# Optimization experiments

Measured on AMD Instinct MI355X. Metric: run time of the kernel, lower is better.

Reference implementation:

```python
import jax, jax.numpy as jnp
import numpy as np

POOL_K = {56: 8, 28: 4, 14: 2, 7: 1}


def _maxpool(x, k):
    # kernel == stride maxpool via reshape-max
    if k == 1:
        return x
    B, C, H, W = x.shape
    return x.reshape(B, C, H // k, k, W // k, k).max(axis=(3, 5))


def _scale(act):
    # act: [B, C, H0, W0] -> pooled [B, C, 7, 7]
    B, C, H0, W0 = act.shape
    p = _maxpool(act, POOL_K[H0]).reshape(B, C, -1)  # [B, C, HW], HW=49
    # heatmap[i,j,e,f] = sum_c p[i,c,e] * p[j,c,f]  -> [B, B, HW, HW]
    heat = jax.nn.softmax(jnp.einsum('ice,jcf->ijef', p, p), axis=-1)
    # out[i,j,e,c] = sum_f heat[i,j,e,f] * p[j,c,f]  -> [B, B, HW, C]
    out = jnp.einsum('ijef,jcf->ijec', heat, p)
    return out, heat


def setup_inputs() -> dict:
    key = jax.random.key(0)
    k1, k2, k3, k4 = jax.random.split(key, 4)
    B = 16
    return {
        'act1': jax.random.normal(k1, (B, 256, 56, 56), dtype=jnp.float32),
        'act2': jax.random.normal(k2, (B, 512, 28, 28), dtype=jnp.float32),
        'act3': jax.random.normal(k3, (B, 1024, 14, 14), dtype=jnp.float32),
        'act4': jax.random.normal(k4, (B, 2048, 7, 7), dtype=jnp.float32),
    }


def reference(act1, act2, act3, act4):
    outs_heats = [_scale(a) for a in (act1, act2, act3, act4)]
    outs = tuple(o for o, _ in outs_heats)
    heats = tuple(h for _, h in outs_heats)
    return outs + heats
```

## Files before the change

### kernel.cpp

```cpp
#include <hip/hip_runtime.h>
#include <hip/hip_bf16.h>
#include <cstdint>
#include <cstddef>


typedef __attribute__((ext_vector_type(8))) short s16x8;
typedef __attribute__((ext_vector_type(4))) float f32x4;

#define SPART 802816

__device__ __forceinline__ unsigned short f2bf(float x) {
    uint32_t u = __float_as_uint(x);
    uint32_t r = (u + 0x7fff + ((u >> 16) & 1)) >> 16;
    return (unsigned short)r;
}
__device__ __forceinline__ float bf2f(unsigned short b) {
    return __uint_as_float(((uint32_t)b) << 16);
}
__device__ __forceinline__ void gll16(const void* g, void* l) {
    __builtin_amdgcn_global_load_lds(
        (const __attribute__((address_space(1))) uint32_t*)g,
        (__attribute__((address_space(3))) uint32_t*)l, 16, 0, 0);
}

__global__ __launch_bounds__(256) void pool_kernel(const float* __restrict__ act,
                                                   unsigned short* __restrict__ Pk,
                                                   unsigned short* __restrict__ Pk2,
                                                   unsigned short* __restrict__ Vb,
                                                   int C, int H, int k, int G) {
    __shared__ float plane[3136];
    const int HW = H * H;
    const int nblk_c = C / G;
    const int i  = blockIdx.x / nblk_c;
    const int c0 = (blockIdx.x % nblk_c) * G;
    const float* src = act + ((size_t)i * C + c0) * HW;
    for (int idx = threadIdx.x; idx < G * HW; idx += 256)
        plane[idx] = src[idx];
    __syncthreads();
    for (int idx = threadIdx.x; idx < G * 49; idx += 256) {
        const int e = idx / G, g = idx % G;
        const int eh = e / 7, ew = e % 7;
        const float* pp = plane + g * HW + (eh * k) * H + ew * k;
        float m = -INFINITY;
        for (int dy = 0; dy < k; ++dy)
            for (int dx = 0; dx < k; ++dx)
                m = fmaxf(m, pp[dy * H + dx]);
        const int c = c0 + g;
        const unsigned short hb = f2bf(m);
        const unsigned short lb = f2bf(m - bf2f(hb));
        const size_t pk = (((size_t)(c >> 2) * 896) + (size_t)i * 56 + e) * 8 + ((c & 3) * 2);
        *reinterpret_cast<uint32_t*>(&Pk[pk])  = (uint32_t)hb | ((uint32_t)lb << 16);
        *reinterpret_cast<uint32_t*>(&Pk2[pk]) = (uint32_t)lb | ((uint32_t)hb << 16);
        const size_t vb = (((size_t)i * 8 + (e >> 3)) * C + c) * 8 + (e & 7);
        Vb[vb] = hb;
    }
    for (int idx = threadIdx.x; idx < 7 * G; idx += 256) {
        const int e = 49 + idx / G, g = idx % G, c = c0 + g;
        const size_t pk = (((size_t)(c >> 2) * 896) + (size_t)i * 56 + e) * 8 + ((c & 3) * 2);
        *reinterpret_cast<uint32_t*>(&Pk[pk])  = 0;
        *reinterpret_cast<uint32_t*>(&Pk2[pk]) = 0;
    }
    for (int idx = threadIdx.x; idx < 15 * G; idx += 256) {
        const int e = 49 + idx / G, g = idx % G, c = c0 + g;
        const size_t vb = (((size_t)i * 8 + (e >> 3)) * C + c) * 8 + (e & 7);
        Vb[vb] = 0;
    }
}

struct GramParams {
    const unsigned short* Pk[4];
    const unsigned short* Pk2[4];
    float* S[4];
    int Kblk[4];
    int cum[5];
};

__global__ __launch_bounds__(256) void gram_kernel(GramParams g) {
    __shared__ short lsA[4 * 128 * 8];
    __shared__ short lsB[4 * 128 * 8];
    __shared__ short lsB2[4 * 128 * 8];
    int b = blockIdx.x, s = 0;
    while (b >= g.cum[s + 1]) s++;
    const int rem = b - g.cum[s];
    const int p = rem / 49, t = rem % 49;
    const int bi = t / 7, bj = t % 7;
    const int Kb = g.Kblk[s];
    const int kg0 = p * (Kb >> 3);
    const unsigned short* __restrict__ Pk  = g.Pk[s];
    const unsigned short* __restrict__ Pk2 = g.Pk2[s];
    float* __restrict__ S = g.S[s] + (size_t)p * SPART;

    const int tid = threadIdx.x, lane = tid & 63, w = tid >> 6;
    const int wm = (w >> 1) * 64, wn = (w & 1) * 64;

    f32x4 acc[4][4];
    #pragma unroll
    for (int u = 0; u < 4; ++u)
        #pragma unroll
        for (int v = 0; v < 4; ++v)
            acc[u][v] = (f32x4){0.f, 0.f, 0.f, 0.f};

    const int half = lane >> 4, r16 = lane & 15;
    for (int it = 0; it < (Kb >> 5); ++it) {
        const int kq = kg0 + it * 4 + w;
        const char* ga  = (const char*)Pk  + ((size_t)kq * 896 + bi * 128) * 16 + lane * 16;
        const char* gb  = (const char*)Pk  + ((size_t)kq * 896 + bj * 128) * 16 + lane * 16;
        const char* gb2 = (const char*)Pk2 + ((size_t)kq * 896 + bj * 128) * 16 + lane * 16;
        gll16(ga,         (char*)lsA  + w * 2048);
        gll16(ga  + 1024, (char*)lsA  + w * 2048 + 1024);
        gll16(gb,         (char*)lsB  + w * 2048);
        gll16(gb  + 1024, (char*)lsB  + w * 2048 + 1024);
        gll16(gb2,        (char*)lsB2 + w * 2048);
        gll16(gb2 + 1024, (char*)lsB2 + w * 2048 + 1024);
        __syncthreads();
        s16x8 av[4], bv[4], cv[4];
        #pragma unroll
        for (int u = 0; u < 4; ++u) {
            av[u] = *reinterpret_cast<const s16x8*>(&lsA [((half * 128) + wm + 16 * u + r16) * 8]);
            bv[u] = *reinterpret_cast<const s16x8*>(&lsB [((half * 128) + wn + 16 * u + r16) * 8]);
            cv[u] = *reinterpret_cast<const s16x8*>(&lsB2[((half * 128) + wn + 16 * u + r16) * 8]);
        }
        #pragma unroll
        for (int u = 0; u < 4; ++u)
            #pragma unroll
            for (int v = 0; v < 4; ++v) {
                acc[u][v] = __builtin_amdgcn_mfma_f32_16x16x32_bf16(av[u], bv[v], acc[u][v], 0, 0, 0);
                acc[u][v] = __builtin_amdgcn_mfma_f32_16x16x32_bf16(av[u], cv[v], acc[u][v], 0, 0, 0);
            }
        __syncthreads();
    }

    const int rowb = bi * 128 + wm + (lane >> 4) * 4;
    const int colb = bj * 128 + wn + (lane & 15);
    #pragma unroll
    for (int u = 0; u < 4; ++u)
        #pragma unroll
        for (int v = 0; v < 4; ++v)
            #pragma unroll
            for (int rg = 0; rg < 4; ++rg)
                S[(size_t)(rowb + 16 * u + rg) * 896 + colb + 16 * v] = acc[u][v][rg];
}

struct SoftParams {
    const float* S[4];
    float* heat[4];
    unsigned short* Hb[4];
    int np[4];
};

__global__ __launch_bounds__(256) void softmax_kernel(SoftParams sp) {
    const int grp = (blockIdx.x * 256 + threadIdx.x) >> 4;
    const int l = threadIdx.x & 15;
    const int s = grp / 12544;
    const int rem = grp % 12544;
    const int i = rem / 784;
    const int j = (rem / 49) % 16;
    const int e = rem % 49;
    const float* __restrict__ Sb = sp.S[s];
    const int np = sp.np[s];
    const size_t rowoff = ((size_t)(i * 56 + e)) * 896 + j * 56;

    float v[4];
    #pragma unroll
    for (int t = 0; t < 4; ++t) {
        const int f = l + t * 16;
        float x = -INFINITY;
        if (f < 49) {
            x = 0.f;
            for (int p = 0; p < np; ++p) x += Sb[(size_t)p * SPART + rowoff + f];
        }
        v[t] = x;
    }
    float m = fmaxf(fmaxf(v[0], v[1]), fmaxf(v[2], v[3]));
    #pragma unroll
    for (int d = 1; d < 16; d <<= 1) m = fmaxf(m, __shfl_xor(m, d, 16));
    float ex[4], sum = 0.f;
    #pragma unroll
    for (int t = 0; t < 4; ++t) {
        const int f = l + t * 16;
        ex[t] = (f < 49) ? __expf(v[t] - m) : 0.f;
        sum += ex[t];
    }
    #pragma unroll
    for (int d = 1; d < 16; d <<= 1) sum += __shfl_xor(sum, d, 16);
    const float inv = 1.f / sum;

    float* hrow = sp.heat[s] + (((size_t)(i * 16 + j)) * 49 + e) * 49;
    unsigned short* __restrict__ Hb = sp.Hb[s];
    const size_t hbrow = (size_t)i * 56 + e;
    #pragma unroll
    for (int t = 0; t < 4; ++t) {
        const int f = l + t * 16;
        const float hv = (f < 49) ? ex[t] * inv : 0.f;
        if (f < 49) hrow[f] = hv;
        Hb[(((size_t)j * 8 + (f >> 3)) * 896 + hbrow) * 8 + (f & 7)] = f2bf(hv);
    }
}

struct PvParams {
    const unsigned short* Hb[4];
    const unsigned short* Vb[4];
    float* out[4];
    int C[4];
    int cum[5];
};

__global__ __launch_bounds__(256) void pv_kernel(PvParams pv) {
    __shared__ short lsA[8 * 128 * 8];
    __shared__ short lsB[8 * 128 * 8];
    int b = blockIdx.x, s = 0;
    while (b >= pv.cum[s + 1]) s++;
    int rem = b - pv.cum[s];
    const int C = pv.C[s], nct = C >> 7;
    const int j = rem / (7 * nct); rem %= 7 * nct;
    const int rt = rem / nct, ct = rem % nct;
    const int tid = threadIdx.x, lane = tid & 63, w = tid >> 6;
    const int wm = (w >> 1) * 64, wn = (w & 1) * 64;
    const unsigned short* __restrict__ Hb = pv.Hb[s];
    const unsigned short* __restrict__ Vb = pv.Vb[s];

    #pragma unroll
    for (int q = 0; q < 2; ++q) {
        const int kq = w + q * 4;
        const char* ga = (const char*)Hb + ((size_t)(j * 8 + kq) * 896 + rt * 128) * 16 + lane * 16;
        const char* gb = (const char*)Vb + ((size_t)(j * 8 + kq) * C + ct * 128) * 16 + lane * 16;
        gll16(ga,        (char*)lsA + kq * 2048);
        gll16(ga + 1024, (char*)lsA + kq * 2048 + 1024);
        gll16(gb,        (char*)lsB + kq * 2048);
        gll16(gb + 1024, (char*)lsB + kq * 2048 + 1024);
    }
    __syncthreads();

    f32x4 acc[4][4];
    #pragma unroll
    for (int u = 0; u < 4; ++u)
        #pragma unroll
        for (int v = 0; v < 4; ++v)
            acc[u][v] = (f32x4){0.f, 0.f, 0.f, 0.f};

    const int r16 = lane & 15;
    #pragma unroll
    for (int ks = 0; ks < 2; ++ks) {
        const int half = ks * 4 + (lane >> 4);
        s16x8 av[4], bv[4];
        #pragma unroll
        for (int u = 0; u < 4; ++u) {
            av[u] = *reinterpret_cast<const s16x8*>(&lsA[((half * 128) + wm + 16 * u + r16) * 8]);
            bv[u] = *reinterpret_cast<const s16x8*>(&lsB[((half * 128) + wn + 16 * u + r16) * 8]);
        }
        #pragma unroll
        for (int u = 0; u < 4; ++u)
            #pragma unroll
            for (int v = 0; v < 4; ++v)
                acc[u][v] = __builtin_amdgcn_mfma_f32_16x16x32_bf16(av[u], bv[v], acc[u][v], 0, 0, 0);
    }

    #pragma unroll
    for (int u = 0; u < 4; ++u) {
        const int mb = rt * 128 + wm + 16 * u + (lane >> 4) * 4;
        #pragma unroll
        for (int rg = 0; rg < 4; ++rg) {
            const int mm = mb + rg;
            const int ii = mm / 56, e = mm % 56;
            if (e < 49) {
                float* orow = pv.out[s] + (((size_t)(ii * 16 + j)) * 49 + e) * C + ct * 128 + (lane & 15);
                #pragma unroll
                for (int v = 0; v < 4; ++v)
                    orow[wn + 16 * v] = acc[u][v][rg];
            }
        }
    }
}

extern "C" void kernel_launch(void* const* d_in, const int* in_sizes, int n_in,
                              void* d_out, int out_size, void* d_ws, size_t ws_size,
                              hipStream_t stream) {
    const float* acts[4] = {(const float*)d_in[0], (const float*)d_in[1],
                            (const float*)d_in[2], (const float*)d_in[3]};
    const int Cs[4] = {256, 512, 1024, 2048};

    char* w0 = (char*)d_ws;
    size_t off = 0;
    unsigned short *Pk[4], *Pk2[4], *Vb[4], *Hb[4];
    for (int s = 0; s < 4; ++s) { Pk[s]  = (unsigned short*)(w0 + off); off += (size_t)3584 * Cs[s]; }
    for (int s = 0; s < 4; ++s) { Pk2[s] = (unsigned short*)(w0 + off); off += (size_t)3584 * Cs[s]; }
    for (int s = 0; s < 4; ++s) { Vb[s]  = (unsigned short*)(w0 + off); off += (size_t)2048 * Cs[s]; }
    for (int s = 0; s < 4; ++s) { Hb[s]  = (unsigned short*)(w0 + off); off += (size_t)1835008; }

    const bool full = ws_size >= off + (size_t)15 * SPART * 4;
    int np[4];
    if (full) { np[0] = 1; np[1] = 2; np[2] = 4; np[3] = 8; }
    else      { np[0] = 1; np[1] = 1; np[2] = 1; np[3] = 1; }
    float* Sp[4];
    for (int s = 0; s < 4; ++s) { Sp[s] = (float*)(w0 + off); off += (size_t)np[s] * SPART * 4; }

    float* out = (float*)d_out;
    const size_t o1 = 0;
    const size_t o2 = o1 + (size_t)256 * 49 * 256;
    const size_t o3 = o2 + (size_t)256 * 49 * 512;
    const size_t o4 = o3 + (size_t)256 * 49 * 1024;
    const size_t h1 = o4 + (size_t)256 * 49 * 2048;
    const size_t h2 = h1 + (size_t)256 * 2401;
    const size_t h3 = h2 + (size_t)256 * 2401;
    const size_t h4 = h3 + (size_t)256 * 2401;
    float* heat[4] = {out + h1, out + h2, out + h3, out + h4};
    float* outs[4] = {out + o1, out + o2, out + o3, out + o4};

    pool_kernel<<<16 * 256, 256, 0, stream>>>(acts[0], Pk[0], Pk2[0], Vb[0], 256, 56, 8, 1);
    pool_kernel<<<16 * 128, 256, 0, stream>>>(acts[1], Pk[1], Pk2[1], Vb[1], 512, 28, 4, 4);
    pool_kernel<<<16 * 64,  256, 0, stream>>>(acts[2], Pk[2], Pk2[2], Vb[2], 1024, 14, 2, 16);
    pool_kernel<<<16 * 32,  256, 0, stream>>>(acts[3], Pk[3], Pk2[3], Vb[3], 2048, 7, 1, 64);

    GramParams g;
    g.cum[0] = 0;
    for (int s = 0; s < 4; ++s) {
        g.Pk[s] = Pk[s];
        g.Pk2[s] = Pk2[s];
        g.S[s] = Sp[s];
        g.Kblk[s] = 2 * Cs[s] / np[s];
        g.cum[s + 1] = g.cum[s] + np[s] * 49;
    }
    gram_kernel<<<g.cum[4], 256, 0, stream>>>(g);

    SoftParams sp;
    for (int s = 0; s < 4; ++s) {
        sp.S[s] = Sp[s]; sp.heat[s] = heat[s]; sp.Hb[s] = Hb[s]; sp.np[s] = np[s];
    }
    softmax_kernel<<<3136, 256, 0, stream>>>(sp);

    PvParams pv;
    pv.cum[0] = 0;
    for (int s = 0; s < 4; ++s) {
        pv.Hb[s] = Hb[s]; pv.Vb[s] = Vb[s]; pv.out[s] = outs[s]; pv.C[s] = Cs[s];
        pv.cum[s + 1] = pv.cum[s] + 16 * 7 * (Cs[s] >> 7);
    }
    pv_kernel<<<pv.cum[4], 256, 0, stream>>>(pv);
}
```

Measured before the change: 164.7 us.

## Merge pool launches, drop Pk2 buffer, reuse V tile across row tiles in PV

```diff
diff --git a/kernel.cpp b/kernel.cpp
--- a/kernel.cpp
+++ b/kernel.cpp
@@ -6,6 +6,7 @@
 
 typedef __attribute__((ext_vector_type(8))) short s16x8;
 typedef __attribute__((ext_vector_type(4))) float f32x4;
+typedef __attribute__((ext_vector_type(4))) uint32_t u32x4;
 
 #define SPART 802816
 
@@ -23,42 +24,51 @@
         (__attribute__((address_space(3))) uint32_t*)l, 16, 0, 0);
 }
 
-__global__ __launch_bounds__(256) void pool_kernel(const float* __restrict__ act,
-                                                   unsigned short* __restrict__ Pk,
-                                                   unsigned short* __restrict__ Pk2,
-                                                   unsigned short* __restrict__ Vb,
-                                                   int C, int H, int k, int G) {
-    __shared__ float plane[3136];
+struct PoolParams {
+    const float* act[4];
+    unsigned short* Pk[4];
+    unsigned short* Vb[4];
+    int C[4], H[4], k[4], G[4], cum[5];
+};
+
+__global__ __launch_bounds__(256) void pool_all_kernel(PoolParams pp) {
+    __shared__ alignas(16) float plane[3136];
+    int b = blockIdx.x, s = 0;
+    while (b >= pp.cum[s + 1]) s++;
+    const int rem = b - pp.cum[s];
+    const int C = pp.C[s], H = pp.H[s], k = pp.k[s], G = pp.G[s];
     const int HW = H * H;
     const int nblk_c = C / G;
-    const int i  = blockIdx.x / nblk_c;
-    const int c0 = (blockIdx.x % nblk_c) * G;
-    const float* src = act + ((size_t)i * C + c0) * HW;
-    for (int idx = threadIdx.x; idx < G * HW; idx += 256)
-        plane[idx] = src[idx];
+    const int i  = rem / nblk_c;
+    const int c0 = (rem % nblk_c) * G;
+    unsigned short* __restrict__ Pk = pp.Pk[s];
+    unsigned short* __restrict__ Vb = pp.Vb[s];
+
+    const float4* src4 = reinterpret_cast<const float4*>(pp.act[s] + ((size_t)i * C + c0) * HW);
+    float4* plane4 = reinterpret_cast<float4*>(plane);
+    for (int idx = threadIdx.x; idx < (G * HW) >> 2; idx += 256)
+        plane4[idx] = src4[idx];
     __syncthreads();
     for (int idx = threadIdx.x; idx < G * 49; idx += 256) {
         const int e = idx / G, g = idx % G;
         const int eh = e / 7, ew = e % 7;
-        const float* pp = plane + g * HW + (eh * k) * H + ew * k;
+        const float* ppl = plane + g * HW + (eh * k) * H + ew * k;
         float m = -INFINITY;
         for (int dy = 0; dy < k; ++dy)
             for (int dx = 0; dx < k; ++dx)
-                m = fmaxf(m, pp[dy * H + dx]);
+                m = fmaxf(m, ppl[dy * H + dx]);
         const int c = c0 + g;
         const unsigned short hb = f2bf(m);
         const unsigned short lb = f2bf(m - bf2f(hb));
         const size_t pk = (((size_t)(c >> 2) * 896) + (size_t)i * 56 + e) * 8 + ((c & 3) * 2);
-        *reinterpret_cast<uint32_t*>(&Pk[pk])  = (uint32_t)hb | ((uint32_t)lb << 16);
-        *reinterpret_cast<uint32_t*>(&Pk2[pk]) = (uint32_t)lb | ((uint32_t)hb << 16);
+        *reinterpret_cast<uint32_t*>(&Pk[pk]) = (uint32_t)hb | ((uint32_t)lb << 16);
         const size_t vb = (((size_t)i * 8 + (e >> 3)) * C + c) * 8 + (e & 7);
         Vb[vb] = hb;
     }
     for (int idx = threadIdx.x; idx < 7 * G; idx += 256) {
         const int e = 49 + idx / G, g = idx % G, c = c0 + g;
         const size_t pk = (((size_t)(c >> 2) * 896) + (size_t)i * 56 + e) * 8 + ((c & 3) * 2);
-        *reinterpret_cast<uint32_t*>(&Pk[pk])  = 0;
-        *reinterpret_cast<uint32_t*>(&Pk2[pk]) = 0;
+        *reinterpret_cast<uint32_t*>(&Pk[pk]) = 0;
     }
     for (int idx = threadIdx.x; idx < 15 * G; idx += 256) {
         const int e = 49 + idx / G, g = idx % G, c = c0 + g;
@@ -69,7 +79,6 @@
 
 struct GramParams {
     const unsigned short* Pk[4];
-    const unsigned short* Pk2[4];
     float* S[4];
     int Kblk[4];
     int cum[5];
@@ -78,7 +87,6 @@
 __global__ __launch_bounds__(256) void gram_kernel(GramParams g) {
     __shared__ short lsA[4 * 128 * 8];
     __shared__ short lsB[4 * 128 * 8];
-    __shared__ short lsB2[4 * 128 * 8];
     int b = blockIdx.x, s = 0;
     while (b >= g.cum[s + 1]) s++;
     const int rem = b - g.cum[s];
@@ -86,8 +94,7 @@
     const int bi = t / 7, bj = t % 7;
     const int Kb = g.Kblk[s];
     const int kg0 = p * (Kb >> 3);
-    const unsigned short* __restrict__ Pk  = g.Pk[s];
-    const unsigned short* __restrict__ Pk2 = g.Pk2[s];
+    const unsigned short* __restrict__ Pk = g.Pk[s];
     float* __restrict__ S = g.S[s] + (size_t)p * SPART;
 
     const int tid = threadIdx.x, lane = tid & 63, w = tid >> 6;
@@ -103,22 +110,22 @@
     const int half = lane >> 4, r16 = lane & 15;
     for (int it = 0; it < (Kb >> 5); ++it) {
         const int kq = kg0 + it * 4 + w;
-        const char* ga  = (const char*)Pk  + ((size_t)kq * 896 + bi * 128) * 16 + lane * 16;
-        const char* gb  = (const char*)Pk  + ((size_t)kq * 896 + bj * 128) * 16 + lane * 16;
-        const char* gb2 = (const char*)Pk2 + ((size_t)kq * 896 + bj * 128) * 16 + lane * 16;
-        gll16(ga,         (char*)lsA  + w * 2048);
-        gll16(ga  + 1024, (char*)lsA  + w * 2048 + 1024);
-        gll16(gb,         (char*)lsB  + w * 2048);
-        gll16(gb  + 1024, (char*)lsB  + w * 2048 + 1024);
-        gll16(gb2,        (char*)lsB2 + w * 2048);
-        gll16(gb2 + 1024, (char*)lsB2 + w * 2048 + 1024);
+        const char* ga = (const char*)Pk + ((size_t)kq * 896 + bi * 128) * 16 + lane * 16;
+        const char* gb = (const char*)Pk + ((size_t)kq * 896 + bj * 128) * 16 + lane * 16;
+        gll16(ga,        (char*)lsA + w * 2048);
+        gll16(ga + 1024, (char*)lsA + w * 2048 + 1024);
+        gll16(gb,        (char*)lsB + w * 2048);
+        gll16(gb + 1024, (char*)lsB + w * 2048 + 1024);
         __syncthreads();
         s16x8 av[4], bv[4], cv[4];
         #pragma unroll
         for (int u = 0; u < 4; ++u) {
-            av[u] = *reinterpret_cast<const s16x8*>(&lsA [((half * 128) + wm + 16 * u + r16) * 8]);
-            bv[u] = *reinterpret_cast<const s16x8*>(&lsB [((half * 128) + wn + 16 * u + r16) * 8]);
-            cv[u] = *reinterpret_cast<const s16x8*>(&lsB2[((half * 128) + wn + 16 * u + r16) * 8]);
+            av[u] = *reinterpret_cast<const s16x8*>(&lsA[((half * 128) + wm + 16 * u + r16) * 8]);
+            union { u32x4 u4; s16x8 s8; } ub, uc;
+            ub.u4 = *reinterpret_cast<const u32x4*>(&lsB[((half * 128) + wn + 16 * u + r16) * 8]);
+            uc.u4 = (ub.u4 >> 16) | (ub.u4 << 16);
+            bv[u] = ub.s8;
+            cv[u] = uc.s8;
         }
         #pragma unroll
         for (int u = 0; u < 4; ++u)
@@ -212,8 +219,8 @@
     while (b >= pv.cum[s + 1]) s++;
     int rem = b - pv.cum[s];
     const int C = pv.C[s], nct = C >> 7;
-    const int j = rem / (7 * nct); rem %= 7 * nct;
-    const int rt = rem / nct, ct = rem % nct;
+    const int j  = rem / (nct * 2); rem %= nct * 2;
+    const int ct = rem >> 1, rh = rem & 1;
     const int tid = threadIdx.x, lane = tid & 63, w = tid >> 6;
     const int wm = (w >> 1) * 64, wn = (w & 1) * 64;
     const unsigned short* __restrict__ Hb = pv.Hb[s];
@@ -222,75 +229,85 @@
     #pragma unroll
     for (int q = 0; q < 2; ++q) {
         const int kq = w + q * 4;
-        const char* ga = (const char*)Hb + ((size_t)(j * 8 + kq) * 896 + rt * 128) * 16 + lane * 16;
         const char* gb = (const char*)Vb + ((size_t)(j * 8 + kq) * C + ct * 128) * 16 + lane * 16;
-        gll16(ga,        (char*)lsA + kq * 2048);
-        gll16(ga + 1024, (char*)lsA + kq * 2048 + 1024);
         gll16(gb,        (char*)lsB + kq * 2048);
         gll16(gb + 1024, (char*)lsB + kq * 2048 + 1024);
     }
-    __syncthreads();
-
-    f32x4 acc[4][4];
-    #pragma unroll
-    for (int u = 0; u < 4; ++u)
-        #pragma unroll
-        for (int v = 0; v < 4; ++v)
-            acc[u][v] = (f32x4){0.f, 0.f, 0.f, 0.f};
 
     const int r16 = lane & 15;
-    #pragma unroll
-    for (int ks = 0; ks < 2; ++ks) {
-        const int half = ks * 4 + (lane >> 4);
-        s16x8 av[4], bv[4];
-        #pragma unroll
-        for (int u = 0; u < 4; ++u) {
-            av[u] = *reinterpret_cast<const s16x8*>(&lsA[((half * 128) + wm + 16 * u + r16) * 8]);
-            bv[u] = *reinterpret_cast<const s16x8*>(&lsB[((half * 128) + wn + 16 * u + r16) * 8]);
-        }
+    for (int rt = rh; rt < 7; rt += 2) {
+        #pragma unroll
+        for (int q = 0; q < 2; ++q) {
+            const int kq = w + q * 4;
+            const char* ga = (const char*)Hb + ((size_t)(j * 8 + kq) * 896 + rt * 128) * 16 + lane * 16;
+            gll16(ga,        (char*)lsA + kq * 2048);
+            gll16(ga + 1024, (char*)lsA + kq * 2048 + 1024);
+        }
+        __syncthreads();
+
+        f32x4 acc[4][4];
         #pragma unroll
         for (int u = 0; u < 4; ++u)
             #pragma unroll
             for (int v = 0; v < 4; ++v)
-                acc[u][v] = __builtin_amdgcn_mfma_f32_16x16x32_bf16(av[u], bv[v], acc[u][v], 0, 0, 0);
-    }
-
-    #pragma unroll
-    for (int u = 0; u < 4; ++u) {
-        const int mb = rt * 128 + wm + 16 * u + (lane >> 4) * 4;
-        #pragma unroll
-        for (int rg = 0; rg < 4; ++rg) {
-            const int mm = mb + rg;
-            const int ii = mm / 56, e = mm % 56;
-            if (e < 49) {
-                float* orow = pv.out[s] + (((size_t)(ii * 16 + j)) * 49 + e) * C + ct * 128 + (lane & 15);
+                acc[u][v] = (f32x4){0.f, 0.f, 0.f, 0.f};
+
+        #pragma unroll
+        for (int ks = 0; ks < 2; ++ks) {
+            const int half = ks * 4 + (lane >> 4);
+            s16x8 av[4], bv[4];
+            #pragma unroll
+            for (int u = 0; u < 4; ++u) {
+                av[u] = *reinterpret_cast<const s16x8*>(&lsA[((half * 128) + wm + 16 * u + r16) * 8]);
+                bv[u] = *reinterpret_cast<const s16x8*>(&lsB[((half * 128) + wn + 16 * u + r16) * 8]);
+            }
+            #pragma unroll
+            for (int u = 0; u < 4; ++u)
                 #pragma unroll
                 for (int v = 0; v < 4; ++v)
-                    orow[wn + 16 * v] = acc[u][v][rg];
+                    acc[u][v] = __builtin_amdgcn_mfma_f32_16x16x32_bf16(av[u], bv[v], acc[u][v], 0, 0, 0);
+        }
+
+        #pragma unroll
+        for (int u = 0; u < 4; ++u) {
+            const int mb = rt * 128 + wm + 16 * u + (lane >> 4) * 4;
+            #pragma unroll
+            for (int rg = 0; rg < 4; ++rg) {
+                const int mm = mb + rg;
+                const int ii = mm / 56, e = mm % 56;
+                if (e < 49) {
+                    float* orow = pv.out[s] + (((size_t)(ii * 16 + j)) * 49 + e) * C + ct * 128 + (lane & 15);
+                    #pragma unroll
+                    for (int v = 0; v < 4; ++v)
+                        orow[wn + 16 * v] = acc[u][v][rg];
+                }
             }
         }
+        __syncthreads();
     }
 }
 
 extern "C" void kernel_launch(void* const* d_in, const int* in_sizes, int n_in,
                               void* d_out, int out_size, void* d_ws, size_t ws_size,
                               hipStream_t stream) {
-    const float* acts[4] = {(const float*)d_in[0], (const float*)d_in[1],
-                            (const float*)d_in[2], (const float*)d_in[3]};
     const int Cs[4] = {256, 512, 1024, 2048};
+    const int Hs[4] = {56, 28, 14, 7};
+    const int ks[4] = {8, 4, 2, 1};
+    const int Gs[4] = {1, 4, 16, 64};
 
     char* w0 = (char*)d_ws;
     size_t off = 0;
-    unsigned short *Pk[4], *Pk2[4], *Vb[4], *Hb[4];
-    for (int s = 0; s < 4; ++s) { Pk[s]  = (unsigned short*)(w0 + off); off += (size_t)3584 * Cs[s]; }
-    for (int s = 0; s < 4; ++s) { Pk2[s] = (unsigned short*)(w0 + off); off += (size_t)3584 * Cs[s]; }
-    for (int s = 0; s < 4; ++s) { Vb[s]  = (unsigned short*)(w0 + off); off += (size_t)2048 * Cs[s]; }
-    for (int s = 0; s < 4; ++s) { Hb[s]  = (unsigned short*)(w0 + off); off += (size_t)1835008; }
-
-    const bool full = ws_size >= off + (size_t)15 * SPART * 4;
-    int np[4];
-    if (full) { np[0] = 1; np[1] = 2; np[2] = 4; np[3] = 8; }
-    else      { np[0] = 1; np[1] = 1; np[2] = 1; np[3] = 1; }
+    unsigned short *Pk[4], *Vb[4], *Hb[4];
+    for (int s = 0; s < 4; ++s) { Pk[s] = (unsigned short*)(w0 + off); off += (size_t)3584 * Cs[s]; }
+    for (int s = 0; s < 4; ++s) { Vb[s] = (unsigned short*)(w0 + off); off += (size_t)2048 * Cs[s]; }
+    for (int s = 0; s < 4; ++s) { Hb[s] = (unsigned short*)(w0 + off); off += (size_t)1835008; }
+
+    int np[4] = {1, 2, 2, 4};
+    {
+        size_t need = off;
+        for (int s = 0; s < 4; ++s) need += (size_t)np[s] * SPART * 4;
+        if (ws_size < need) { np[0] = np[1] = np[2] = np[3] = 1; }
+    }
     float* Sp[4];
     for (int s = 0; s < 4; ++s) { Sp[s] = (float*)(w0 + off); off += (size_t)np[s] * SPART * 4; }
 
@@ -306,16 +323,20 @@
     float* heat[4] = {out + h1, out + h2, out + h3, out + h4};
     float* outs[4] = {out + o1, out + o2, out + o3, out + o4};
 
-    pool_kernel<<<16 * 256, 256, 0, stream>>>(acts[0], Pk[0], Pk2[0], Vb[0], 256, 56, 8, 1);
-    pool_kernel<<<16 * 128, 256, 0, stream>>>(acts[1], Pk[1], Pk2[1], Vb[1], 512, 28, 4, 4);
-    pool_kernel<<<16 * 64,  256, 0, stream>>>(acts[2], Pk[2], Pk2[2], Vb[2], 1024, 14, 2, 16);
-    pool_kernel<<<16 * 32,  256, 0, stream>>>(acts[3], Pk[3], Pk2[3], Vb[3], 2048, 7, 1, 64);
+    PoolParams pp;
+    pp.cum[0] = 0;
+    for (int s = 0; s < 4; ++s) {
+        pp.act[s] = (const float*)d_in[s];
+        pp.Pk[s] = Pk[s]; pp.Vb[s] = Vb[s];
+        pp.C[s] = Cs[s]; pp.H[s] = Hs[s]; pp.k[s] = ks[s]; pp.G[s] = Gs[s];
+        pp.cum[s + 1] = pp.cum[s] + 16 * (Cs[s] / Gs[s]);
+    }
+    pool_all_kernel<<<pp.cum[4], 256, 0, stream>>>(pp);
 
     GramParams g;
     g.cum[0] = 0;
     for (int s = 0; s < 4; ++s) {
         g.Pk[s] = Pk[s];
-        g.Pk2[s] = Pk2[s];
         g.S[s] = Sp[s];
         g.Kblk[s] = 2 * Cs[s] / np[s];
         g.cum[s + 1] = g.cum[s] + np[s] * 49;
@@ -332,7 +353,7 @@
     pv.cum[0] = 0;
     for (int s = 0; s < 4; ++s) {
         pv.Hb[s] = Hb[s]; pv.Vb[s] = Vb[s]; pv.out[s] = outs[s]; pv.C[s] = Cs[s];
-        pv.cum[s + 1] = pv.cum[s] + 16 * 7 * (Cs[s] >> 7);
+        pv.cum[s + 1] = pv.cum[s] + 16 * (Cs[s] >> 7) * 2;
     }
     pv_kernel<<<pv.cum[4], 256, 0, stream>>>(pv);
 }
```

Result: faster. 135.6 us (-17.7%).
